# Kernel tuning notes

Hardware: AMD Instinct MI355X
Metric: run time of the kernel (lower is better)

The kernel has to match this reference:

```python
import jax, jax.numpy as jnp
import numpy as np

B, S, D = 2, 2048, 1024   # batch, seq, d_model
E, F, K = 8, 2048, 2      # num_experts, ffn_hidden_size, top_k


def setup_inputs() -> dict:
    key = jax.random.key(0)
    ks = jax.random.split(key, 5)
    scale = 0.02
    hidden_states = jax.random.normal(ks[0], (B, S, D), dtype=jnp.float32)
    router_kernel = jax.random.normal(ks[1], (D, E), dtype=jnp.float32) * scale
    # expert params, already reshaped to (E, F, D) as in DbrxExpertGLU.expert_shape
    w1 = jax.random.normal(ks[2], (E, F, D), dtype=jnp.float32) * scale
    v1 = jax.random.normal(ks[3], (E, F, D), dtype=jnp.float32) * scale
    w2 = jax.random.normal(ks[4], (E, F, D), dtype=jnp.float32) * scale
    return {"hidden_states": hidden_states, "router_kernel": router_kernel,
            "w1": w1, "v1": v1, "w2": w2}


def reference(hidden_states, router_kernel, w1, v1, w2):
    # ---- Router ----
    logits = jnp.einsum('bsd,de->bse', hidden_states.astype(jnp.float32), router_kernel)
    weights = jax.nn.softmax(logits, axis=-1)                # [B,S,E]
    top_weights, top_experts = jax.lax.top_k(weights, K)     # [B,S,K]
    # moe_normalize_expert_weights = 1 -> L1 normalization
    top_weights = top_weights / jnp.sum(jnp.abs(top_weights), axis=-1, keepdims=True)
    weights = weights.astype(hidden_states.dtype)
    top_weights = top_weights.astype(hidden_states.dtype)
    # ---- Experts: every expert's GLU over all tokens, masked accumulation ----
    out = jnp.zeros_like(hidden_states)
    for e in range(E):  # small fixed expert count; matches original loop
        x1 = jnp.einsum('bsd,fd->bsf', hidden_states, w1[e])   # [B,S,F]
        x2 = jnp.einsum('bsd,fd->bsf', hidden_states, v1[e])
        h = jax.nn.silu(x1) * x2
        y_e = jnp.einsum('bsf,fd->bsd', h, w2[e])               # [B,S,D]
        gate = jnp.sum((top_experts == e) * top_weights, axis=-1)  # [B,S]
        out = out + gate[:, :, None] * y_e
    return out, weights
```

## Files before the change

### kernel.cpp

```cpp
#include <hip/hip_runtime.h>
#include <stdint.h>
#include <math.h>

#define NB 2
#define NS 2048
#define ND 1024
#define NE 8
#define NF 2048
#define NTOK (NB*NS)
#define EFD ((size_t)NE*NF*ND)
#define NROWS (2*NTOK)

typedef short bf16x8 __attribute__((ext_vector_type(8)));
typedef float f32x4 __attribute__((ext_vector_type(4)));

__device__ __forceinline__ unsigned short f2bf(float f) {
  unsigned u = __float_as_uint(f);
  unsigned r = (u + 0x7FFFu + ((u >> 16) & 1u)) >> 16;
  return (unsigned short)r;
}
__device__ __forceinline__ float bf2f(unsigned short s) {
  return __uint_as_float(((unsigned)s) << 16);
}

__device__ __forceinline__ void async16(unsigned short* lds, const unsigned short* g) {
  __builtin_amdgcn_global_load_lds(
      (const __attribute__((address_space(1))) unsigned int*)g,
      (__attribute__((address_space(3))) unsigned int*)lds, 16, 0, 0);
}

#define VMCNT(n) asm volatile("s_waitcnt vmcnt(" #n ")" ::: "memory")
#define LGKM0    asm volatile("s_waitcnt lgkmcnt(0)" ::: "memory")
#define SBAR     __builtin_amdgcn_s_barrier()
#define SCHED0   __builtin_amdgcn_sched_barrier(0)

__global__ void cvt_bf16(const float* __restrict__ src,
                         unsigned short* __restrict__ dst, int n4) {
  int i = blockIdx.x * blockDim.x + threadIdx.x;
  int stride = gridDim.x * blockDim.x;
  for (; i < n4; i += stride) {
    float4 v = ((const float4*)src)[i];
    ushort4 o;
    o.x = f2bf(v.x); o.y = f2bf(v.y); o.z = f2bf(v.z); o.w = f2bf(v.w);
    ((ushort4*)dst)[i] = o;
  }
}

__global__ void transpose_w2(const float* __restrict__ w2,
                             unsigned short* __restrict__ w2t) {
  __shared__ float tile[32][33];
  int e = blockIdx.z;
  int d0 = blockIdx.x * 32, f0 = blockIdx.y * 32;
  int tx = threadIdx.x, ty = threadIdx.y;
  const float* src = w2 + (size_t)e * NF * ND;
  unsigned short* dst = w2t + (size_t)e * ND * NF;
#pragma unroll
  for (int i = ty; i < 32; i += 8)
    tile[i][tx] = src[(size_t)(f0 + i) * ND + d0 + tx];
  __syncthreads();
#pragma unroll
  for (int i = ty; i < 32; i += 8)
    dst[(size_t)(d0 + i) * NF + f0 + tx] = f2bf(tile[tx][i]);
}

__global__ void router_kernel(const float* __restrict__ hs,
                              const float* __restrict__ rk,
                              float* __restrict__ wout,
                              float* __restrict__ tw,
                              int* __restrict__ choice,
                              unsigned short* __restrict__ hsb) {
  int lane = threadIdx.x;
  int tt = lane & 15, part = lane >> 4;
  int t = blockIdx.x * 16 + tt;
  const float4* hrow = (const float4*)(hs + (size_t)t * ND) + part * 64;
  ushort4* hb4 = (ushort4*)(hsb + (size_t)t * ND) + part * 64;
  const float4* rk4 = (const float4*)rk + part * 512;
  float acc[NE];
#pragma unroll
  for (int e = 0; e < NE; ++e) acc[e] = 0.f;
#pragma unroll 4
  for (int i = 0; i < 64; ++i) {
    float4 x = hrow[i];
    ushort4 o;
    o.x = f2bf(x.x); o.y = f2bf(x.y); o.z = f2bf(x.z); o.w = f2bf(x.w);
    hb4[i] = o;
    float xs[4] = {x.x, x.y, x.z, x.w};
#pragma unroll
    for (int j = 0; j < 4; ++j) {
      float4 r0 = rk4[i * 8 + j * 2];
      float4 r1 = rk4[i * 8 + j * 2 + 1];
      acc[0] += xs[j] * r0.x; acc[1] += xs[j] * r0.y;
      acc[2] += xs[j] * r0.z; acc[3] += xs[j] * r0.w;
      acc[4] += xs[j] * r1.x; acc[5] += xs[j] * r1.y;
      acc[6] += xs[j] * r1.z; acc[7] += xs[j] * r1.w;
    }
  }
#pragma unroll
  for (int e = 0; e < NE; ++e) {
    acc[e] += __shfl_xor(acc[e], 16, 64);
    acc[e] += __shfl_xor(acc[e], 32, 64);
  }
  if (part == 0) {
    float mx = acc[0]; int i0 = 0;
#pragma unroll
    for (int e = 1; e < NE; ++e) if (acc[e] > mx) { mx = acc[e]; i0 = e; }
    float m2 = -3.4e38f; int i1 = 0;
#pragma unroll
    for (int e = 0; e < NE; ++e) if (e != i0 && acc[e] > m2) { m2 = acc[e]; i1 = e; }
    float p[NE]; float den = 0.f;
#pragma unroll
    for (int e = 0; e < NE; ++e) { p[e] = expf(acc[e] - mx); den += p[e]; }
    float inv = 1.f / den;
#pragma unroll
    for (int e = 0; e < NE; ++e) { p[e] *= inv; wout[t * NE + e] = p[e]; }
    float w0 = p[i0], w1 = p[i1];
    float s = 1.f / (w0 + w1);
    tw[t * 2 + 0] = w0 * s;
    tw[t * 2 + 1] = w1 * s;
    choice[t] = i0 | (i1 << 4);
  }
}

__global__ void build_lists(const int* __restrict__ choice,
                            int* __restrict__ counts,
                            int* __restrict__ off,
                            int* __restrict__ list,
                            int* __restrict__ posn) {
  __shared__ int lcnt[NE];
  int tid = threadIdx.x;
  if (tid < NE) lcnt[tid] = 0;
  __syncthreads();
  int4 c4 = ((const int4*)choice)[tid];
  int cs[4] = {c4.x, c4.y, c4.z, c4.w};
#pragma unroll
  for (int j = 0; j < 4; ++j) {
    int t = tid * 4 + j;
    int e0 = cs[j] & 15, e1 = (cs[j] >> 4) & 15;
    int p0 = atomicAdd(&lcnt[e0], 1);
    list[e0 * NTOK + p0] = t << 1;
    int p1 = atomicAdd(&lcnt[e1], 1);
    list[e1 * NTOK + p1] = (t << 1) | 1;
    posn[t] = p0 | (p1 << 16);
  }
  __syncthreads();
  if (tid == 0) {
    int s = 0;
#pragma unroll
    for (int e = 0; e < NE; ++e) { counts[e] = lcnt[e]; off[e] = s; s += lcnt[e]; }
    off[NE] = s;
  }
}

__global__ __launch_bounds__(256, 2) void gemm_fused(
    const int* __restrict__ counts, const int* __restrict__ off,
    const int* __restrict__ list,
    const unsigned short* __restrict__ A,
    const unsigned short* __restrict__ B1,
    const unsigned short* __restrict__ B2,
    unsigned short* __restrict__ H) {
  int bid = blockIdx.x;
  int e = bid >> 9;
  int rem = bid & 511;
  int mt = rem >> 4, nt = rem & 15;
  int cnt = counts[e];
  if (mt * 128 >= cnt) return;
  int off_e = off[e];

  __shared__ unsigned short lds[2][12288];

  int tid = threadIdx.x;
  int wid = tid >> 6, lane = tid & 63;
  int wr = wid >> 1, wc = wid & 1;
  int l15 = lane & 15, l4 = lane >> 4;
  const int* mylist = list + e * NTOK;

  int trow = tid >> 2;
  int co = ((tid & 3) ^ ((tid >> 3) & 3)) * 8;
  const unsigned short* aS0;
  const unsigned short* aS1;
  {
    int r0 = mt * 128 + trow;
    int r1 = r0 + 64;
    if (r0 >= cnt) r0 = cnt - 1;
    if (r1 >= cnt) r1 = cnt - 1;
    int e0 = mylist[r0], e1 = mylist[r1];
    aS0 = A + (size_t)(e0 >> 1) * ND + co;
    aS1 = A + (size_t)(e1 >> 1) * ND + co;
  }
  const unsigned short* b1S0 = B1 + (size_t)e * NF * ND + (size_t)(nt * 128 + trow) * ND + co;
  const unsigned short* b1S1 = b1S0 + (size_t)64 * ND;
  const unsigned short* b2S0 = B2 + (size_t)e * NF * ND + (size_t)(nt * 128 + trow) * ND + co;
  const unsigned short* b2S1 = b2S0 + (size_t)64 * ND;

  int rowA[4], rowB[4];
#pragma unroll
  for (int mi = 0; mi < 4; ++mi) {
    int r = wr * 64 + mi * 16 + l15;
    rowA[mi] = r * 64 + ((l4 ^ ((r >> 1) & 3)) << 4);
  }
#pragma unroll
  for (int ni = 0; ni < 4; ++ni) {
    int r = wc * 64 + ni * 16 + l15;
    rowB[ni] = r * 64 + ((l4 ^ ((r >> 1) & 3)) << 4);
  }

  f32x4 acc1[4][4], acc2[4][4];
#pragma unroll
  for (int mi = 0; mi < 4; ++mi)
#pragma unroll
    for (int ni = 0; ni < 4; ++ni) {
      f32x4 z = {0.f, 0.f, 0.f, 0.f};
      acc1[mi][ni] = z; acc2[mi][ni] = z;
    }

  auto STAGE = [&](int c, int kt) {
    int ko = kt * 32;
    unsigned short* base = &lds[c][0] + tid * 8;
    async16(base,         aS0 + ko);
    async16(base + 2048,  aS1 + ko);
    async16(base + 4096,  b1S0 + ko);
    async16(base + 6144,  b1S1 + ko);
    async16(base + 8192,  b2S0 + ko);
    async16(base + 10240, b2S1 + ko);
  };

  const int kT = ND / 32;
  STAGE(0, 0); STAGE(1, 1);

  for (int kt = 0; kt < kT; ++kt) {
    int cur = kt & 1;
    if (kt + 1 < kT) { VMCNT(6); }
    else             { VMCNT(0); }
    SCHED0;
    SBAR;

    const char* la = (const char*)&lds[cur][0];
    const char* lb1 = la + 8192;
    const char* lb2 = la + 16384;
    bf16x8 a[4], b1[4], b2[4];
#pragma unroll
    for (int mi = 0; mi < 4; ++mi)
      a[mi] = *(const bf16x8*)(la + rowA[mi]);
#pragma unroll
    for (int ni = 0; ni < 4; ++ni) {
      b1[ni] = *(const bf16x8*)(lb1 + rowB[ni]);
      b2[ni] = *(const bf16x8*)(lb2 + rowB[ni]);
    }
    LGKM0;
    SCHED0;
    SBAR;
    if (kt + 2 < kT) STAGE(cur, kt + 2);

    __builtin_amdgcn_s_setprio(1);
#pragma unroll
    for (int mi = 0; mi < 4; ++mi)
#pragma unroll
      for (int ni = 0; ni < 4; ++ni) {
        acc1[mi][ni] = __builtin_amdgcn_mfma_f32_16x16x32_bf16(
            a[mi], b1[ni], acc1[mi][ni], 0, 0, 0);
        acc2[mi][ni] = __builtin_amdgcn_mfma_f32_16x16x32_bf16(
            a[mi], b2[ni], acc2[mi][ni], 0, 0, 0);
      }
    __builtin_amdgcn_s_setprio(0);
  }

  int rowbase = mt * 128 + wr * 64;
  int colbase = nt * 128 + wc * 64;
#pragma unroll
  for (int mi = 0; mi < 4; ++mi) {
#pragma unroll
    for (int j = 0; j < 4; ++j) {
      int r = rowbase + mi * 16 + l4 * 4 + j;
      if (r >= cnt) continue;
      size_t row = (size_t)(off_e + r);
#pragma unroll
      for (int ni = 0; ni < 4; ++ni) {
        int c = colbase + ni * 16 + l15;
        float x1 = acc1[mi][ni][j];
        float x2 = acc2[mi][ni][j];
        float h = (x1 / (1.f + expf(-x1))) * x2;
        H[row * NF + c] = f2bf(h);
      }
    }
  }
}

__global__ __launch_bounds__(256, 2) void gemm_p3(
    const int* __restrict__ counts, const int* __restrict__ off,
    const unsigned short* __restrict__ Ah,
    const unsigned short* __restrict__ Bw,
    unsigned short* __restrict__ Y) {
  int bid = blockIdx.x;
  int e = bid >> 8;
  int rem = bid & 255;
  int mt = rem >> 3;
  int code = rem & 7;
  int nt = code >> 1, kh = code & 1;
  int cnt = counts[e];
  if (mt * 128 >= cnt) return;
  int off_e = off[e];

  __shared__ unsigned short lds[2][12288];

  int tid = threadIdx.x;
  int wid = tid >> 6, lane = tid & 63;
  int wr = wid >> 1, wc = wid & 1;
  int l15 = lane & 15, l4 = lane >> 4;

  int trow = tid >> 2;
  int co = ((tid & 3) ^ ((tid >> 3) & 3)) * 8;
  const unsigned short* aS[2];
#pragma unroll
  for (int g = 0; g < 2; ++g) {
    int r = mt * 128 + g * 64 + trow;
    if (r >= cnt) r = cnt - 1;
    aS[g] = Ah + (size_t)(off_e + r) * NF + kh * 1024 + co;
  }
  const unsigned short* bS[4];
#pragma unroll
  for (int g = 0; g < 4; ++g) {
    int d = nt * 256 + g * 64 + trow;
    bS[g] = Bw + (size_t)e * ND * NF + (size_t)d * NF + kh * 1024 + co;
  }

  int rowA[4], rowB[8];
#pragma unroll
  for (int mi = 0; mi < 4; ++mi) {
    int r = wr * 64 + mi * 16 + l15;
    rowA[mi] = r * 64 + ((l4 ^ ((r >> 1) & 3)) << 4);
  }
#pragma unroll
  for (int ni = 0; ni < 8; ++ni) {
    int r = wc * 128 + ni * 16 + l15;
    rowB[ni] = 8192 + r * 64 + ((l4 ^ ((r >> 1) & 3)) << 4);
  }

  f32x4 acc[4][8];
#pragma unroll
  for (int mi = 0; mi < 4; ++mi)
#pragma unroll
    for (int ni = 0; ni < 8; ++ni) {
      f32x4 z = {0.f, 0.f, 0.f, 0.f};
      acc[mi][ni] = z;
    }

  auto STAGE = [&](int c, int kt) {
    int ko = kt * 32;
    unsigned short* base = &lds[c][0] + tid * 8;
    async16(base,         aS[0] + ko);
    async16(base + 2048,  aS[1] + ko);
    async16(base + 4096,  bS[0] + ko);
    async16(base + 6144,  bS[1] + ko);
    async16(base + 8192,  bS[2] + ko);
    async16(base + 10240, bS[3] + ko);
  };

  const int kT = 32;
  STAGE(0, 0); STAGE(1, 1);

  for (int kt = 0; kt < kT; ++kt) {
    int cur = kt & 1;
    if (kt + 1 < kT) { VMCNT(6); }
    else             { VMCNT(0); }
    SCHED0;
    SBAR;

    const char* buf = (const char*)&lds[cur][0];
    bf16x8 a[4], b[8];
#pragma unroll
    for (int mi = 0; mi < 4; ++mi)
      a[mi] = *(const bf16x8*)(buf + rowA[mi]);
#pragma unroll
    for (int ni = 0; ni < 8; ++ni)
      b[ni] = *(const bf16x8*)(buf + rowB[ni]);
    LGKM0;
    SCHED0;
    SBAR;
    if (kt + 2 < kT) STAGE(cur, kt + 2);

    __builtin_amdgcn_s_setprio(1);
#pragma unroll
    for (int mi = 0; mi < 4; ++mi)
#pragma unroll
      for (int ni = 0; ni < 8; ++ni)
        acc[mi][ni] = __builtin_amdgcn_mfma_f32_16x16x32_bf16(
            a[mi], b[ni], acc[mi][ni], 0, 0, 0);
    __builtin_amdgcn_s_setprio(0);
  }

  unsigned short* Yp = Y + (size_t)kh * NROWS * ND;
#pragma unroll
  for (int mi = 0; mi < 4; ++mi)
#pragma unroll
    for (int j = 0; j < 4; ++j) {
      int r = mt * 128 + wr * 64 + mi * 16 + l4 * 4 + j;
      if (r >= cnt) continue;
      size_t row = (size_t)(off_e + r);
#pragma unroll
      for (int ni = 0; ni < 8; ++ni) {
        int d = nt * 256 + wc * 128 + ni * 16 + l15;
        Yp[row * ND + d] = f2bf(acc[mi][ni][j]);
      }
    }
}

__global__ void combine_kernel(const unsigned short* __restrict__ yc,
                               const float* __restrict__ tw,
                               const int* __restrict__ choice,
                               const int* __restrict__ posn,
                               const int* __restrict__ off,
                               float* __restrict__ out) {
  int t = blockIdx.x;
  int tid = threadIdx.x;
  int ch = choice[t];
  int pp = posn[t];
  int e0 = ch & 15, e1 = (ch >> 4) & 15;
  size_t r0 = (size_t)(off[e0] + (pp & 0xffff));
  size_t r1 = (size_t)(off[e1] + (pp >> 16));
  float w0 = tw[t * 2], w1 = tw[t * 2 + 1];
  const size_t P = (size_t)NROWS * ND;
  ushort4 a0 = ((const ushort4*)(yc + r0 * ND))[tid];
  ushort4 b0 = ((const ushort4*)(yc + P + r0 * ND))[tid];
  ushort4 a1 = ((const ushort4*)(yc + r1 * ND))[tid];
  ushort4 b1 = ((const ushort4*)(yc + P + r1 * ND))[tid];
  float4 o;
  o.x = w0 * (bf2f(a0.x) + bf2f(b0.x)) + w1 * (bf2f(a1.x) + bf2f(b1.x));
  o.y = w0 * (bf2f(a0.y) + bf2f(b0.y)) + w1 * (bf2f(a1.y) + bf2f(b1.y));
  o.z = w0 * (bf2f(a0.z) + bf2f(b0.z)) + w1 * (bf2f(a1.z) + bf2f(b1.z));
  o.w = w0 * (bf2f(a0.w) + bf2f(b0.w)) + w1 * (bf2f(a1.w) + bf2f(b1.w));
  ((float4*)(out + (size_t)t * ND))[tid] = o;
}


extern "C" void kernel_launch(void* const* d_in, const int* in_sizes, int n_in,
                              void* d_out, int out_size, void* d_ws, size_t ws_size,
                              hipStream_t stream) {
  const float* hs = (const float*)d_in[0];
  const float* rk = (const float*)d_in[1];
  const float* w1 = (const float*)d_in[2];
  const float* v1 = (const float*)d_in[3];
  const float* w2 = (const float*)d_in[4];
  float* out = (float*)d_out;
  float* wout = out + (size_t)NTOK * ND;

  char* ws = (char*)d_ws;
  int* counts = (int*)(ws + 0);
  int* off = (int*)(ws + 64);
  int* choice = (int*)(ws + 128);
  int* posn = (int*)(ws + 16512);
  float* tw = (float*)(ws + 32896);
  int* list = (int*)(ws + 65664);
  unsigned short* hsb = (unsigned short*)(ws + 196736);
  unsigned short* w1b = (unsigned short*)(ws + 8585344);
  unsigned short* v1b = (unsigned short*)(ws + 42139776);
  unsigned short* w2t = (unsigned short*)(ws + 75694208);
  unsigned short* hcomp = (unsigned short*)(ws + 109248640);
  unsigned short* ycomp = (unsigned short*)(ws + 142803072);

  router_kernel<<<256, 64, 0, stream>>>(hs, rk, wout, tw, choice, hsb);
  build_lists<<<1, 1024, 0, stream>>>(choice, counts, off, list, posn);

  cvt_bf16<<<4096, 256, 0, stream>>>(w1, w1b, (int)(EFD / 4));
  cvt_bf16<<<4096, 256, 0, stream>>>(v1, v1b, (int)(EFD / 4));
  transpose_w2<<<dim3(ND / 32, NF / 32, NE), dim3(32, 8), 0, stream>>>(w2, w2t);

  gemm_fused<<<4096, 256, 0, stream>>>(counts, off, list, hsb, w1b, v1b, hcomp);

  gemm_p3<<<2048, 256, 0, stream>>>(counts, off, hcomp, w2t, ycomp);

  combine_kernel<<<NTOK, 256, 0, stream>>>(ycomp, tw, choice, posn, off, out);
}
```

Baseline: 271.4 us.

## Merge weight conversions, vectorize w2 transpose, spread router across more blocks

The separate w1 and v1 fp32→bf16 conversion launches become one kernel writing a single contiguous buffer. This relies on v1b sitting directly after w1b in the workspace. The w2 transpose moves to 64x64 tiles with float4 global loads and 16-byte bf16 stores, replacing 2-byte scattered stores. The router now handles 4 tokens per block with coalesced interleaved reads, launching 1024 blocks instead of 256 for better occupancy, at the cost of a longer shuffle reduction.

```diff
diff --git a/kernel.cpp b/kernel.cpp
--- a/kernel.cpp
+++ b/kernel.cpp
@@ -12,6 +12,7 @@
 #define NROWS (2*NTOK)
 
 typedef short bf16x8 __attribute__((ext_vector_type(8)));
+typedef unsigned short u16x8 __attribute__((ext_vector_type(8)));
 typedef float f32x4 __attribute__((ext_vector_type(4)));
 
 __device__ __forceinline__ unsigned short f2bf(float f) {
@@ -34,12 +35,16 @@
 #define SBAR     __builtin_amdgcn_s_barrier()
 #define SCHED0   __builtin_amdgcn_sched_barrier(0)
 
-__global__ void cvt_bf16(const float* __restrict__ src,
-                         unsigned short* __restrict__ dst, int n4) {
+__global__ void cvt_bf16_2(const float* __restrict__ s1,
+                           const float* __restrict__ s2,
+                           unsigned short* __restrict__ dst, int n4each) {
   int i = blockIdx.x * blockDim.x + threadIdx.x;
   int stride = gridDim.x * blockDim.x;
-  for (; i < n4; i += stride) {
-    float4 v = ((const float4*)src)[i];
+  int total = 2 * n4each;
+  for (; i < total; i += stride) {
+    const float4* src = (i < n4each) ? (const float4*)s1 : (const float4*)s2;
+    int k = (i < n4each) ? i : i - n4each;
+    float4 v = src[k];
     ushort4 o;
     o.x = f2bf(v.x); o.y = f2bf(v.y); o.z = f2bf(v.z); o.w = f2bf(v.w);
     ((ushort4*)dst)[i] = o;
@@ -48,19 +53,33 @@
 
 __global__ void transpose_w2(const float* __restrict__ w2,
                              unsigned short* __restrict__ w2t) {
-  __shared__ float tile[32][33];
+  __shared__ float tile[64][65];
   int e = blockIdx.z;
-  int d0 = blockIdx.x * 32, f0 = blockIdx.y * 32;
-  int tx = threadIdx.x, ty = threadIdx.y;
+  int d0 = blockIdx.x * 64, f0 = blockIdx.y * 64;
+  int tid = threadIdx.x;
   const float* src = w2 + (size_t)e * NF * ND;
   unsigned short* dst = w2t + (size_t)e * ND * NF;
-#pragma unroll
-  for (int i = ty; i < 32; i += 8)
-    tile[i][tx] = src[(size_t)(f0 + i) * ND + d0 + tx];
+  int c4 = tid & 15;
+#pragma unroll
+  for (int i = 0; i < 4; ++i) {
+    int fr = (tid >> 4) + i * 16;
+    float4 v = *(const float4*)(src + (size_t)(f0 + fr) * ND + d0 + c4 * 4);
+    tile[fr][c4 * 4 + 0] = v.x;
+    tile[fr][c4 * 4 + 1] = v.y;
+    tile[fr][c4 * 4 + 2] = v.z;
+    tile[fr][c4 * 4 + 3] = v.w;
+  }
   __syncthreads();
-#pragma unroll
-  for (int i = ty; i < 32; i += 8)
-    dst[(size_t)(d0 + i) * NF + f0 + tx] = f2bf(tile[tx][i]);
+  int f8 = tid & 7;
+#pragma unroll
+  for (int i = 0; i < 2; ++i) {
+    int dr = (tid >> 3) + i * 32;
+    u16x8 o;
+#pragma unroll
+    for (int k = 0; k < 8; ++k)
+      o[k] = f2bf(tile[f8 * 8 + k][dr]);
+    *(u16x8*)(dst + (size_t)(d0 + dr) * NF + f0 + f8 * 8) = o;
+  }
 }
 
 __global__ void router_kernel(const float* __restrict__ hs,
@@ -70,25 +89,27 @@
                               int* __restrict__ choice,
                               unsigned short* __restrict__ hsb) {
   int lane = threadIdx.x;
-  int tt = lane & 15, part = lane >> 4;
-  int t = blockIdx.x * 16 + tt;
-  const float4* hrow = (const float4*)(hs + (size_t)t * ND) + part * 64;
-  ushort4* hb4 = (ushort4*)(hsb + (size_t)t * ND) + part * 64;
-  const float4* rk4 = (const float4*)rk + part * 512;
+  int tt = lane >> 4, part = lane & 15;
+  int t = blockIdx.x * 4 + tt;
+  const float4* hrow = (const float4*)(hs + (size_t)t * ND);
+  ushort4* hb4 = (ushort4*)(hsb + (size_t)t * ND);
+  const float4* rk4 = (const float4*)rk;
   float acc[NE];
 #pragma unroll
   for (int e = 0; e < NE; ++e) acc[e] = 0.f;
 #pragma unroll 4
-  for (int i = 0; i < 64; ++i) {
-    float4 x = hrow[i];
+  for (int i = 0; i < 16; ++i) {
+    int fi = part + i * 16;
+    float4 x = hrow[fi];
     ushort4 o;
     o.x = f2bf(x.x); o.y = f2bf(x.y); o.z = f2bf(x.z); o.w = f2bf(x.w);
-    hb4[i] = o;
+    hb4[fi] = o;
     float xs[4] = {x.x, x.y, x.z, x.w};
 #pragma unroll
     for (int j = 0; j < 4; ++j) {
-      float4 r0 = rk4[i * 8 + j * 2];
-      float4 r1 = rk4[i * 8 + j * 2 + 1];
+      int d = fi * 4 + j;
+      float4 r0 = rk4[d * 2];
+      float4 r1 = rk4[d * 2 + 1];
       acc[0] += xs[j] * r0.x; acc[1] += xs[j] * r0.y;
       acc[2] += xs[j] * r0.z; acc[3] += xs[j] * r0.w;
       acc[4] += xs[j] * r1.x; acc[5] += xs[j] * r1.y;
@@ -96,9 +117,9 @@
     }
   }
 #pragma unroll
-  for (int e = 0; e < NE; ++e) {
-    acc[e] += __shfl_xor(acc[e], 16, 64);
-    acc[e] += __shfl_xor(acc[e], 32, 64);
+  for (int m = 1; m <= 8; m <<= 1) {
+#pragma unroll
+    for (int e = 0; e < NE; ++e) acc[e] += __shfl_xor(acc[e], m, 64);
   }
   if (part == 0) {
     float mx = acc[0]; int i0 = 0;
@@ -456,13 +477,13 @@
   unsigned short* w2t = (unsigned short*)(ws + 75694208);
   unsigned short* hcomp = (unsigned short*)(ws + 109248640);
   unsigned short* ycomp = (unsigned short*)(ws + 142803072);
-
-  router_kernel<<<256, 64, 0, stream>>>(hs, rk, wout, tw, choice, hsb);
+  (void)v1b;
+
+  router_kernel<<<NTOK / 4, 64, 0, stream>>>(hs, rk, wout, tw, choice, hsb);
   build_lists<<<1, 1024, 0, stream>>>(choice, counts, off, list, posn);
 
-  cvt_bf16<<<4096, 256, 0, stream>>>(w1, w1b, (int)(EFD / 4));
-  cvt_bf16<<<4096, 256, 0, stream>>>(v1, v1b, (int)(EFD / 4));
-  transpose_w2<<<dim3(ND / 32, NF / 32, NE), dim3(32, 8), 0, stream>>>(w2, w2t);
+  cvt_bf16_2<<<4096, 256, 0, stream>>>(w1, v1, w1b, (int)(EFD / 4));
+  transpose_w2<<<dim3(ND / 64, NF / 64, NE), 256, 0, stream>>>(w2, w2t);
 
   gemm_fused<<<4096, 256, 0, stream>>>(counts, off, list, hsb, w1b, v1b, hcomp);
 
```

New measurement: 239.1 us. -11.9%, faster.
